# Kernel tuning notes

Measured on AMD Instinct MI355X. Metric: run time of the kernel, lower is better.

The kernel has to match this reference:

```python
import jax, jax.numpy as jnp
import numpy as np

N = 100000
E = 1600000
F_IN = 100
H = 64
C = 18
K = 2  # num_stacks
T = 2  # num_layers


def setup_inputs() -> dict:
    key = jax.random.key(0)
    ks = jax.random.split(key, 12)
    def glorot(k, shape):
        fan = shape[-2] + shape[-1]
        s = jnp.sqrt(6.0 / fan)
        return jax.random.uniform(k, shape, jnp.float32, -s, s)
    return {
        "x": jax.random.normal(ks[0], (N, F_IN), jnp.float32),
        "edge_index": jax.random.randint(ks[1], (2, E), 0, N, jnp.int64),
        "init_w1": glorot(ks[2], (K, F_IN, H)),
        "w1": glorot(ks[3], (K, H, H)),
        "root_w1": glorot(ks[4], (K, F_IN, H)),
        "b1": jnp.zeros((K, 1, H), jnp.float32),
        "init_w2": glorot(ks[5], (K, H, C)),
        "w2": glorot(ks[6], (K, C, C)),
        "root_w2": glorot(ks[7], (K, H, C)),
        "b2": jnp.zeros((K, 1, C), jnp.float32),
    }


def _gcn_norm(src, tgt):
    # symmetric normalization, no self loops (PyG ARMAConv default)
    deg = jax.ops.segment_sum(jnp.ones((E,), jnp.float32), tgt, num_segments=N)
    dis = jnp.where(deg > 0, jax.lax.rsqrt(jnp.maximum(deg, 1.0)), 0.0)
    return dis[src] * dis[tgt]  # [E]


def _arma_conv(x, src, tgt, norm, init_w, w, root_w, b):
    # x: [N, Fin]; returns [N, Fout]
    root = jnp.einsum('nf,kfh->knh', x, root_w)  # [K, N, Fout] (shared across layers)
    out = None
    for t in range(T):
        if t == 0:
            h = jnp.einsum('nf,kfh->knh', x, init_w)
        else:
            h = jnp.einsum('knh,khg->kng', out, w)
        # gather-scale-scatter propagation per stack
        msgs = h[:, src, :] * norm[None, :, None]  # [K, E, Fout]
        agg = jax.vmap(lambda m: jax.ops.segment_sum(m, tgt, num_segments=N))(msgs)
        out = jax.nn.relu(agg + root + b)
    return out.mean(axis=0)  # mean over stacks


def reference(x, edge_index, init_w1, w1, root_w1, b1, init_w2, w2, root_w2, b2):
    src, tgt = edge_index[0], edge_index[1]
    norm = _gcn_norm(src, tgt)
    h = jax.nn.relu(_arma_conv(x, src, tgt, norm, init_w1, w1, root_w1, b1))
    out = _arma_conv(h, src, tgt, norm, init_w2, w2, root_w2, b2)
    return jax.nn.log_softmax(out, axis=-1)
```

## Files before the change

kernel.cpp:

```cpp
#include <hip/hip_runtime.h>
#include <hip/hip_bf16.h>
#include <math.h>

#define N_NODES 100000
#define N_EDGES 1600000
#define F_IN 100
#define H 64
#define C 18
#define BSHIFT 8
#define BSIZE 256
#define NBUCKETS ((N_NODES + BSIZE - 1) >> BSHIFT)
#define NBLK 256
#define CHUNK (N_EDGES / NBLK)

typedef __attribute__((ext_vector_type(8))) short v8s;
typedef __attribute__((ext_vector_type(4))) float v4f;
typedef __attribute__((ext_vector_type(2))) float v2f;


__device__ __forceinline__ unsigned bf16_rne(float f) {
    unsigned u = __float_as_uint(f);
    return (u + 0x7FFFu + ((u >> 16) & 1u)) >> 16;
}
__device__ __forceinline__ unsigned pack_bf2(float a, float b) {
    return bf16_rne(a) | (bf16_rne(b) << 16);
}
__device__ __forceinline__ float2 unpack_bf2(unsigned u) {
    return make_float2(__uint_as_float(u << 16), __uint_as_float(u & 0xFFFF0000u));
}
__device__ __forceinline__ ushort pack_fp8x2(float a, float b) {
    int r = __builtin_amdgcn_cvt_pk_fp8_f32(a, b, 0, false);
    return (ushort)(r & 0xFFFF);
}
__device__ __forceinline__ float2 unpack_fp8x2(ushort u) {
    v2f r = __builtin_amdgcn_cvt_pk_f32_fp8((int)u, false);
    return make_float2(r[0], r[1]);
}


__global__ void scan1_kernel(const int* __restrict__ cnt, int* __restrict__ excl,
                             int* __restrict__ bsum, int n) {
    __shared__ int tmp[256];
    int t = threadIdx.x;
    int i = blockIdx.x * 256 + t;
    int v = (i < n) ? cnt[i] : 0;
    tmp[t] = v;
    __syncthreads();
    for (int off = 1; off < 256; off <<= 1) {
        int xv = (t >= off) ? tmp[t - off] : 0;
        __syncthreads();
        tmp[t] += xv;
        __syncthreads();
    }
    if (i < n) excl[i] = tmp[t] - v;
    if (t == 255) bsum[blockIdx.x] = tmp[255];
}

__global__ void __launch_bounds__(512) scan2p_prep_kernel(
        int* __restrict__ bsum, int nb,
        const float* __restrict__ iw1, const float* __restrict__ rw1,
        const float* __restrict__ w1,  const float* __restrict__ iw2,
        const float* __restrict__ rw2, const float* __restrict__ w2,
        ushort* __restrict__ W1T, ushort* __restrict__ WmT,
        ushort* __restrict__ W2T, ushort* __restrict__ W3T) {
    int t = threadIdx.x;
    if (blockIdx.x == 0) {
        __shared__ int s[512];
        int v = (t < nb) ? bsum[t] : 0;
        s[t] = v;
        __syncthreads();
        for (int off = 1; off < 512; off <<= 1) {
            int xv = (t >= off) ? s[t - off] : 0;
            __syncthreads();
            s[t] += xv;
            __syncthreads();
        }
        if (t < nb) bsum[t] = s[t] - v;
        return;
    }
    int gid = (blockIdx.x - 1) * 512 + t;
    if (gid < 32768) {
        int idx = gid;
        int m = idx >> 13, nn = (idx >> 7) & 63, kk = idx & 127;
        int stk = m & 1, isWr = m >> 1;
        float v = 0.f;
        if (kk < F_IN) v = (isWr ? rw1 : iw1)[((size_t)stk * F_IN + kk) * 64 + nn];
        W1T[idx] = (ushort)bf16_rne(v);
    } else if (gid < 32768 + 8192) {
        int idx = gid - 32768;
        int stk = idx >> 12, g = (idx >> 6) & 63, f = idx & 63;
        WmT[idx] = (ushort)bf16_rne(w1[((size_t)stk * 64 + f) * 64 + g]);
    } else if (gid < 32768 + 8192 + 8192) {
        int idx = gid - 32768 - 8192;
        int m = idx >> 11, col = (idx >> 6) & 31, k = idx & 63;
        int stk = m & 1, isWr = m >> 1;
        float v = 0.f;
        if (col < C) v = (isWr ? rw2 : iw2)[((size_t)stk * H + k) * C + col];
        W2T[idx] = (ushort)bf16_rne(v);
    } else if (gid < 32768 + 8192 + 8192 + 2048) {
        int idx = gid - 32768 - 8192 - 8192;
        int stk = idx >> 10, col = (idx >> 5) & 31, k = idx & 31;
        float v = 0.f;
        if (col < C && k < C) v = w2[((size_t)stk * C + k) * C + col];
        W3T[idx] = (ushort)bf16_rne(v);
    }
}

__global__ void scan3_kernel(int* __restrict__ arr, const int* __restrict__ bsum,
                             int n, int sent) {
    int i = blockIdx.x * 256 + threadIdx.x;
    if (i < n) arr[i] += bsum[i >> 8];
    if (i == n && sent >= 0) arr[n] = sent;
}


__global__ void __launch_bounds__(256) histA_kernel(const int* __restrict__ tgt,
                                                    int* __restrict__ hist) {
    __shared__ int h[NBUCKETS];
    int blk = blockIdx.x, t = threadIdx.x;
    for (int i = t; i < NBUCKETS; i += 256) h[i] = 0;
    __syncthreads();
    int e0 = blk * CHUNK, e1 = e0 + CHUNK;
    for (int e = e0 + t; e < e1; e += 256) atomicAdd(&h[tgt[e] >> BSHIFT], 1);
    __syncthreads();
    for (int i = t; i < NBUCKETS; i += 256) hist[i * NBLK + blk] = h[i];
}

__global__ void __launch_bounds__(256) scatterC_kernel(
        const int* __restrict__ src, const int* __restrict__ tgt,
        const int* __restrict__ histx, unsigned* __restrict__ tmp) {
    __shared__ int cur[NBUCKETS];
    int blk = blockIdx.x, t = threadIdx.x;
    for (int i = t; i < NBUCKETS; i += 256) cur[i] = histx[i * NBLK + blk];
    __syncthreads();
    int e0 = blk * CHUNK, e1 = e0 + CHUNK;
    for (int e = e0 + t; e < e1; e += 256) {
        int s = src[e], tg = tgt[e];
        int b = tg >> BSHIFT;
        int pos = atomicAdd(&cur[b], 1);
        tmp[pos] = (unsigned)s | ((unsigned)(tg & (BSIZE - 1)) << 17);
    }
}

__global__ void __launch_bounds__(256) bucketD2_kernel(
        const unsigned* __restrict__ tmp, const int* __restrict__ histx,
        int* __restrict__ rp, float* __restrict__ dinv, int* __restrict__ ssrc) {
    __shared__ int cnt_l[BSIZE];
    __shared__ int scan_l[BSIZE];
    int b = blockIdx.x;
    int t = threadIdx.x;
    int e_lo = histx[(size_t)b * NBLK];
    int e_hi = (b + 1 < NBUCKETS) ? histx[(size_t)(b + 1) * NBLK] : N_EDGES;
    int n_lo = b << BSHIFT;
    int n_hi = min(n_lo + BSIZE, N_NODES);
    int nn = n_hi - n_lo;
    cnt_l[t] = 0;
    __syncthreads();
    for (int e = e_lo + t; e < e_hi; e += 256)
        atomicAdd(&cnt_l[(int)(tmp[e] >> 17)], 1);
    __syncthreads();
    int v = cnt_l[t];
    scan_l[t] = v;
    __syncthreads();
    for (int off = 1; off < 256; off <<= 1) {
        int xv = (t >= off) ? scan_l[t - off] : 0;
        __syncthreads();
        scan_l[t] += xv;
        __syncthreads();
    }
    int my_start = e_lo + scan_l[t] - v;
    if (t < nn) {
        rp[n_lo + t] = my_start;
        dinv[n_lo + t] = (v > 0) ? rsqrtf((float)v) : 0.f;
    }
    if (b == NBUCKETS - 1 && t == 0) rp[N_NODES] = N_EDGES;
    __syncthreads();
    cnt_l[t] = my_start;
    __syncthreads();
    for (int e = e_lo + t; e < e_hi; e += 256) {
        unsigned p = tmp[e];
        int s = (int)(p & 0x1FFFFu);
        int tl = (int)(p >> 17);
        int pos = atomicAdd(&cnt_l[tl], 1);
        ssrc[pos] = s;
    }
}


__global__ void __launch_bounds__(256) dense1_mfma(
        const float* __restrict__ x, const ushort* __restrict__ W1T,
        const float* __restrict__ dinv,
        ushort* __restrict__ g, unsigned* __restrict__ root) {
    __shared__ char xs[64 * 256];
    int tid = threadIdx.x;
    int b0 = blockIdx.x * 64;
    for (int i = tid; i < 4096; i += 256) {
        int row = i >> 6, pr = i & 63;
        int grow = b0 + row;
        unsigned pv = 0;
        if (grow < N_NODES && 2 * pr < F_IN) {
            float v0 = x[(size_t)grow * F_IN + 2 * pr];
            float v1 = (2 * pr + 1 < F_IN) ? x[(size_t)grow * F_IN + 2 * pr + 1] : 0.f;
            pv = pack_bf2(v0, v1);
        }
        int gr = (pr >> 2) ^ (row & 7);
        *(unsigned*)(xs + row * 256 + (gr << 4) + (pr & 3) * 4) = pv;
    }
    __syncthreads();
    int lane = tid & 63;
    int w = __builtin_amdgcn_readfirstlane(tid >> 6);
    int q = lane >> 4, cl = lane & 15;
    int isWr = w >> 1;
    int colbase = (w & 1) * 32;
    v8s bfr[2][2][4];
    #pragma unroll
    for (int stk = 0; stk < 2; ++stk)
        #pragma unroll
        for (int nt = 0; nt < 2; ++nt)
            #pragma unroll
            for (int ks = 0; ks < 4; ++ks) {
                const ushort* p = W1T + ((size_t)(isWr * 2 + stk) * 64 + colbase + nt * 16 + cl) * 128
                                  + ks * 32 + q * 8;
                bfr[stk][nt][ks] = *(const v8s*)p;
            }
    #pragma unroll
    for (int mt = 0; mt < 4; ++mt) {
        v8s afr[4];
        #pragma unroll
        for (int ks = 0; ks < 4; ++ks) {
            int row = mt * 16 + cl;
            int gr = (ks * 4 + q) ^ (row & 7);
            afr[ks] = *(const v8s*)(xs + row * 256 + (gr << 4));
        }
        v4f acc[2][2];
        #pragma unroll
        for (int stk = 0; stk < 2; ++stk)
            #pragma unroll
            for (int nt = 0; nt < 2; ++nt) {
                v4f a = {0.f, 0.f, 0.f, 0.f};
                #pragma unroll
                for (int ks = 0; ks < 4; ++ks)
                    a = __builtin_amdgcn_mfma_f32_16x16x32_bf16(afr[ks], bfr[stk][nt][ks], a, 0, 0, 0);
                acc[stk][nt] = a;
            }
        #pragma unroll
        for (int nt = 0; nt < 2; ++nt)
            #pragma unroll
            for (int reg = 0; reg < 4; ++reg) {
                int node = b0 + mt * 16 + q * 4 + reg;
                if (node < N_NODES) {
                    int col = colbase + nt * 16 + cl;
                    if (isWr == 0) {
                        float dv = dinv[node];
                        g[(size_t)node * 64 + col] = pack_fp8x2(dv * acc[0][nt][reg], dv * acc[1][nt][reg]);
                    } else {
                        root[(size_t)node * 64 + col] = pack_bf2(acc[0][nt][reg], acc[1][nt][reg]);
                    }
                }
            }
    }
}

__global__ void __launch_bounds__(256) dense_mid_mfma(
        const ushort* __restrict__ hk0, const ushort* __restrict__ hk1,
        const ushort* __restrict__ WmT, const float* __restrict__ dinv,
        ushort* __restrict__ g2) {
    __shared__ char hs[2 * 64 * 128];
    int tid = threadIdx.x;
    int b0 = blockIdx.x * 64;
    for (int i = tid; i < 1024; i += 256) {
        int stk = i >> 9, rem = i & 511, row = rem >> 3, gr = rem & 7;
        int grow = b0 + row;
        uint4 v = make_uint4(0, 0, 0, 0);
        const ushort* srcp = stk ? hk1 : hk0;
        if (grow < N_NODES) v = *(const uint4*)(srcp + (size_t)grow * 64 + gr * 8);
        *(uint4*)(hs + stk * 8192 + row * 128 + ((gr ^ (row & 7)) << 4)) = v;
    }
    __syncthreads();
    int lane = tid & 63;
    int w = __builtin_amdgcn_readfirstlane(tid >> 6);
    int q = lane >> 4, cl = lane & 15;
    v8s bfr[2][2];
    #pragma unroll
    for (int stk = 0; stk < 2; ++stk)
        #pragma unroll
        for (int ks = 0; ks < 2; ++ks)
            bfr[stk][ks] = *(const v8s*)(WmT + ((size_t)stk * 64 + w * 16 + cl) * 64 + ks * 32 + q * 8);
    #pragma unroll
    for (int mt = 0; mt < 4; ++mt) {
        v4f acc[2];
        #pragma unroll
        for (int stk = 0; stk < 2; ++stk) {
            v4f a = {0.f, 0.f, 0.f, 0.f};
            #pragma unroll
            for (int ks = 0; ks < 2; ++ks) {
                int row = mt * 16 + cl;
                int gr = (ks * 4 + q) ^ (row & 7);
                v8s af = *(const v8s*)(hs + stk * 8192 + row * 128 + (gr << 4));
                a = __builtin_amdgcn_mfma_f32_16x16x32_bf16(af, bfr[stk][ks], a, 0, 0, 0);
            }
            acc[stk] = a;
        }
        #pragma unroll
        for (int reg = 0; reg < 4; ++reg) {
            int node = b0 + mt * 16 + q * 4 + reg;
            if (node < N_NODES) {
                float dv = dinv[node];
                g2[(size_t)node * 64 + w * 16 + cl] = pack_fp8x2(dv * acc[0][reg], dv * acc[1][reg]);
            }
        }
    }
}

__global__ void __launch_bounds__(256) dense_y2_mfma(
        const ushort* __restrict__ yb, const ushort* __restrict__ W2T,
        const float* __restrict__ dinv,
        unsigned* __restrict__ h2, unsigned* __restrict__ root2) {
    __shared__ char ys[64 * 128];
    int tid = threadIdx.x;
    int b0 = blockIdx.x * 64;
    for (int i = tid; i < 512; i += 256) {
        int row = i >> 3, gr = i & 7;
        int grow = b0 + row;
        uint4 v = make_uint4(0, 0, 0, 0);
        if (grow < N_NODES) v = *(const uint4*)(yb + (size_t)grow * 64 + gr * 8);
        *(uint4*)(ys + row * 128 + ((gr ^ (row & 7)) << 4)) = v;
    }
    __syncthreads();
    int lane = tid & 63;
    int w = __builtin_amdgcn_readfirstlane(tid >> 6);
    int q = lane >> 4, cl = lane & 15;
    int isWr = w >> 1;
    int mbase = (w & 1) * 2;
    v8s bfr[2][2][2];
    #pragma unroll
    for (int stk = 0; stk < 2; ++stk)
        #pragma unroll
        for (int nt = 0; nt < 2; ++nt)
            #pragma unroll
            for (int ks = 0; ks < 2; ++ks)
                bfr[stk][nt][ks] = *(const v8s*)(W2T + ((size_t)(isWr * 2 + stk) * 32 + nt * 16 + cl) * 64
                                                 + ks * 32 + q * 8);
    #pragma unroll
    for (int mi = 0; mi < 2; ++mi) {
        int mt = mbase + mi;
        v8s afr[2];
        #pragma unroll
        for (int ks = 0; ks < 2; ++ks) {
            int row = mt * 16 + cl;
            int gr = (ks * 4 + q) ^ (row & 7);
            afr[ks] = *(const v8s*)(ys + row * 128 + (gr << 4));
        }
        v4f acc[2][2];
        #pragma unroll
        for (int stk = 0; stk < 2; ++stk)
            #pragma unroll
            for (int nt = 0; nt < 2; ++nt) {
                v4f a = {0.f, 0.f, 0.f, 0.f};
                #pragma unroll
                for (int ks = 0; ks < 2; ++ks)
                    a = __builtin_amdgcn_mfma_f32_16x16x32_bf16(afr[ks], bfr[stk][nt][ks], a, 0, 0, 0);
                acc[stk][nt] = a;
            }
        #pragma unroll
        for (int nt = 0; nt < 2; ++nt)
            #pragma unroll
            for (int reg = 0; reg < 4; ++reg) {
                int node = b0 + mt * 16 + q * 4 + reg;
                int col = nt * 16 + cl;
                if (node < N_NODES && col < C) {
                    if (isWr == 0) {
                        float dv = dinv[node];
                        h2[(size_t)node * C + col] = pack_bf2(dv * acc[0][nt][reg], dv * acc[1][nt][reg]);
                    } else {
                        root2[(size_t)node * C + col] = pack_bf2(acc[0][nt][reg], acc[1][nt][reg]);
                    }
                }
            }
    }
}

__global__ void __launch_bounds__(256) dense_last_mfma(
        const ushort* __restrict__ ok0, const ushort* __restrict__ ok1,
        const ushort* __restrict__ W3T, const float* __restrict__ dinv,
        unsigned* __restrict__ h3) {
    __shared__ char hs[2 * 64 * 64];
    int tid = threadIdx.x;
    int b0 = blockIdx.x * 64;
    for (int i = tid; i < 2048; i += 256) ((unsigned*)hs)[i] = 0;
    __syncthreads();
    for (int i = tid; i < 4096; i += 256) {
        int stk = i >> 11, row = (i >> 5) & 63, col = i & 31;
        int node = b0 + row;
        if (col < C && node < N_NODES) {
            ushort v = (stk ? ok1 : ok0)[(size_t)node * C + col];
            int gr = (col >> 3) ^ (row & 3);
            *(ushort*)(hs + stk * 4096 + row * 64 + (gr << 4) + (col & 7) * 2) = v;
        }
    }
    __syncthreads();
    int lane = tid & 63;
    int w = __builtin_amdgcn_readfirstlane(tid >> 6);
    int q = lane >> 4, cl = lane & 15;
    v8s bfr[2][2];
    #pragma unroll
    for (int stk = 0; stk < 2; ++stk)
        #pragma unroll
        for (int nt = 0; nt < 2; ++nt)
            bfr[stk][nt] = *(const v8s*)(W3T + ((size_t)stk * 32 + nt * 16 + cl) * 32 + q * 8);
    int row = w * 16 + cl;
    int gr = q ^ (row & 3);
    v8s af0 = *(const v8s*)(hs + row * 64 + (gr << 4));
    v8s af1 = *(const v8s*)(hs + 4096 + row * 64 + (gr << 4));
    v4f acc[2][2];
    #pragma unroll
    for (int nt = 0; nt < 2; ++nt) {
        acc[0][nt] = __builtin_amdgcn_mfma_f32_16x16x32_bf16(af0, bfr[0][nt], (v4f){0.f,0.f,0.f,0.f}, 0, 0, 0);
        acc[1][nt] = __builtin_amdgcn_mfma_f32_16x16x32_bf16(af1, bfr[1][nt], (v4f){0.f,0.f,0.f,0.f}, 0, 0, 0);
    }
    #pragma unroll
    for (int nt = 0; nt < 2; ++nt)
        #pragma unroll
        for (int reg = 0; reg < 4; ++reg) {
            int node = b0 + w * 16 + q * 4 + reg;
            int col = nt * 16 + cl;
            if (node < N_NODES && col < C) {
                float dv = dinv[node];
                h3[(size_t)node * C + col] = pack_bf2(dv * acc[0][nt][reg], dv * acc[1][nt][reg]);
            }
        }
}


template <int FINAL>
__global__ void __launch_bounds__(256) prop64_kernel(
        const ushort* __restrict__ g, const unsigned* __restrict__ root,
        const float* __restrict__ b, const float* __restrict__ dinv,
        const int* __restrict__ rp, const int* __restrict__ ssrc,
        ushort* __restrict__ ok0, ushort* __restrict__ ok1, ushort* __restrict__ yb) {
    int lane = threadIdx.x & 63;
    int wid = __builtin_amdgcn_readfirstlane((int)((blockIdx.x * 256 + threadIdx.x) >> 6));
    if (wid >= N_NODES) return;
    int e0 = rp[wid], e1 = rp[wid + 1];
    float a0 = 0.f, a1 = 0.f;
    int e = e0;
    for (; e + 8 <= e1; e += 8) {
        ushort u[8];
        #pragma unroll
        for (int j = 0; j < 8; ++j) u[j] = g[(size_t)ssrc[e + j] * H + lane];
        #pragma unroll
        for (int j = 0; j < 8; ++j) { float2 v = unpack_fp8x2(u[j]); a0 += v.x; a1 += v.y; }
    }
    for (; e < e1; ++e) {
        float2 v = unpack_fp8x2(g[(size_t)ssrc[e] * H + lane]);
        a0 += v.x; a1 += v.y;
    }
    float dv = dinv[wid];
    float2 rt = unpack_bf2(root[(size_t)wid * H + lane]);
    float o0 = fmaxf(fmaf(dv, a0, rt.x + b[lane]), 0.f);
    float o1 = fmaxf(fmaf(dv, a1, rt.y + b[H + lane]), 0.f);
    if (FINAL) {
        yb[(size_t)wid * H + lane] = (ushort)bf16_rne(0.5f * (o0 + o1));
    } else {
        ok0[(size_t)wid * H + lane] = (ushort)bf16_rne(o0);
        ok1[(size_t)wid * H + lane] = (ushort)bf16_rne(o1);
    }
}

template <int FINAL>
__global__ void __launch_bounds__(256) prop18_kernel(
        const unsigned* __restrict__ g, const unsigned* __restrict__ root,
        const float* __restrict__ b, const float* __restrict__ dinv,
        const int* __restrict__ rp, const int* __restrict__ ssrc,
        ushort* __restrict__ ok0, ushort* __restrict__ ok1, float* __restrict__ outp) {
    int lane = threadIdx.x & 63;
    int wid = __builtin_amdgcn_readfirstlane((int)((blockIdx.x * 256 + threadIdx.x) >> 6));
    if (wid >= N_NODES) return;
    int e0 = rp[wid], e1 = rp[wid + 1];
    bool act = lane < C;
    int c = act ? lane : 0;
    float a0 = 0.f, a1 = 0.f;
    int e = e0;
    for (; e + 8 <= e1; e += 8) {
        unsigned u[8];
        #pragma unroll
        for (int j = 0; j < 8; ++j) u[j] = g[(size_t)ssrc[e + j] * C + c];
        if (act) {
            #pragma unroll
            for (int j = 0; j < 8; ++j) { float2 v = unpack_bf2(u[j]); a0 += v.x; a1 += v.y; }
        }
    }
    for (; e < e1; ++e) {
        float2 v = unpack_bf2(g[(size_t)ssrc[e] * C + c]);
        if (act) { a0 += v.x; a1 += v.y; }
    }
    float dv = dinv[wid];
    if (!FINAL) {
        if (act) {
            float2 rt = unpack_bf2(root[(size_t)wid * C + c]);
            float o0 = fmaxf(fmaf(dv, a0, rt.x + b[c]), 0.f);
            float o1 = fmaxf(fmaf(dv, a1, rt.y + b[C + c]), 0.f);
            ok0[(size_t)wid * C + c] = (ushort)bf16_rne(o0);
            ok1[(size_t)wid * C + c] = (ushort)bf16_rne(o1);
        }
    } else {
        float m = -INFINITY;
        if (act) {
            float2 rt = unpack_bf2(root[(size_t)wid * C + c]);
            float o0 = fmaxf(fmaf(dv, a0, rt.x + b[c]), 0.f);
            float o1 = fmaxf(fmaf(dv, a1, rt.y + b[C + c]), 0.f);
            m = 0.5f * (o0 + o1);
        }
        float mx = m;
        #pragma unroll
        for (int off = 16; off >= 1; off >>= 1) mx = fmaxf(mx, __shfl_xor(mx, off, 64));
        float ex = act ? __expf(m - mx) : 0.f;
        float sum = ex;
        #pragma unroll
        for (int off = 16; off >= 1; off >>= 1) sum += __shfl_xor(sum, off, 64);
        if (act) outp[(size_t)wid * C + c] = m - mx - logf(sum);
    }
}


extern "C" void kernel_launch(void* const* d_in, const int* in_sizes, int n_in,
                              void* d_out, int out_size, void* d_ws, size_t ws_size,
                              hipStream_t stream) {
    const float* x        = (const float*)d_in[0];
    const int*   ei       = (const int*)d_in[1];
    const float* init_w1  = (const float*)d_in[2];
    const float* w1       = (const float*)d_in[3];
    const float* root_w1  = (const float*)d_in[4];
    const float* b1       = (const float*)d_in[5];
    const float* init_w2  = (const float*)d_in[6];
    const float* w2       = (const float*)d_in[7];
    const float* root_w2  = (const float*)d_in[8];
    const float* b2       = (const float*)d_in[9];
    const int* src = ei;
    const int* tgt = ei + N_EDGES;
    float* out = (float*)d_out;

    char* w = (char*)d_ws;
    size_t off = 0;
    auto alloc = [&](size_t bytes) -> char* {
        char* p = w + off;
        off += (bytes + 255) & ~(size_t)255;
        return p;
    };
    int*      rp    = (int*)alloc((size_t)(N_NODES + 1) * 4);
    float*    dinv  = (float*)alloc((size_t)N_NODES * 4);
    int*      bsum  = (int*)alloc(512 * 4);
    int*      hist  = (int*)alloc((size_t)NBUCKETS * NBLK * 4);
    int*      histx = (int*)alloc((size_t)NBUCKETS * NBLK * 4);
    unsigned* tmp   = (unsigned*)alloc((size_t)N_EDGES * 4);
    int*      ssrc  = (int*)alloc((size_t)N_EDGES * 4);
    ushort*   W1T   = (ushort*)alloc((size_t)4 * 64 * 128 * 2);
    ushort*   WmT   = (ushort*)alloc((size_t)2 * 64 * 64 * 2);
    ushort*   W2T   = (ushort*)alloc((size_t)4 * 32 * 64 * 2);
    ushort*   W3T   = (ushort*)alloc((size_t)2 * 32 * 32 * 2);
    ushort*   g1    = (ushort*)alloc((size_t)N_NODES * H * 2);
    unsigned* root1 = (unsigned*)alloc((size_t)N_NODES * H * 4);
    ushort*   hk0   = (ushort*)alloc((size_t)N_NODES * H * 2);
    ushort*   hk1   = (ushort*)alloc((size_t)N_NODES * H * 2);
    ushort*   g2    = (ushort*)alloc((size_t)N_NODES * H * 2);
    ushort*   yb    = (ushort*)alloc((size_t)N_NODES * H * 2);
    unsigned* l2buf = (unsigned*)alloc((size_t)3 * N_NODES * C * 4);
    unsigned* h2u    = l2buf;
    unsigned* root2u = l2buf + (size_t)N_NODES * C;
    unsigned* h3u    = l2buf + (size_t)2 * N_NODES * C;
    ushort*   p18k0  = (ushort*)root1;
    ushort*   p18k1  = (ushort*)root1 + (size_t)N_NODES * C;

    int nbH = (NBUCKETS * NBLK + 255) / 256;

    histA_kernel<<<NBLK, 256, 0, stream>>>(tgt, hist);
    scan1_kernel<<<nbH, 256, 0, stream>>>(hist, histx, bsum, NBUCKETS * NBLK);
    scan2p_prep_kernel<<<101, 512, 0, stream>>>(bsum, nbH,
                                                init_w1, root_w1, w1, init_w2, root_w2, w2,
                                                W1T, WmT, W2T, W3T);
    scan3_kernel<<<nbH, 256, 0, stream>>>(histx, bsum, NBUCKETS * NBLK, -1);
    scatterC_kernel<<<NBLK, 256, 0, stream>>>(src, tgt, histx, tmp);
    bucketD2_kernel<<<NBUCKETS, 256, 0, stream>>>(tmp, histx, rp, dinv, ssrc);

    int gblocks = (N_NODES + 63) / 64;
    int pgrid   = (N_NODES + 3) / 4;

    dense1_mfma<<<gblocks, 256, 0, stream>>>(x, W1T, dinv, g1, root1);
    prop64_kernel<0><<<pgrid, 256, 0, stream>>>(g1, root1, b1, dinv, rp, ssrc, hk0, hk1, nullptr);
    dense_mid_mfma<<<gblocks, 256, 0, stream>>>(hk0, hk1, WmT, dinv, g2);
    prop64_kernel<1><<<pgrid, 256, 0, stream>>>(g2, root1, b1, dinv, rp, ssrc, nullptr, nullptr, yb);

    dense_y2_mfma<<<gblocks, 256, 0, stream>>>(yb, W2T, dinv, h2u, root2u);
    prop18_kernel<0><<<pgrid, 256, 0, stream>>>(h2u, root2u, b2, dinv, rp, ssrc, p18k0, p18k1, nullptr);
    dense_last_mfma<<<gblocks, 256, 0, stream>>>(p18k0, p18k1, W3T, dinv, h3u);
    prop18_kernel<1><<<pgrid, 256, 0, stream>>>(h3u, root2u, b2, dinv, rp, ssrc, nullptr, nullptr, out);
}
```

Before: 332.0 us.

## Store 18-wide layer-2 messages as fp8 pairs and split edges across half-waves

```diff
diff --git a/kernel.cpp b/kernel.cpp
--- a/kernel.cpp
+++ b/kernel.cpp
@@ -315,7 +315,7 @@
 __global__ void __launch_bounds__(256) dense_y2_mfma(
         const ushort* __restrict__ yb, const ushort* __restrict__ W2T,
         const float* __restrict__ dinv,
-        unsigned* __restrict__ h2, unsigned* __restrict__ root2) {
+        ushort* __restrict__ h2, unsigned* __restrict__ root2) {
     __shared__ char ys[64 * 128];
     int tid = threadIdx.x;
     int b0 = blockIdx.x * 64;
@@ -371,7 +371,7 @@
                 if (node < N_NODES && col < C) {
                     if (isWr == 0) {
                         float dv = dinv[node];
-                        h2[(size_t)node * C + col] = pack_bf2(dv * acc[0][nt][reg], dv * acc[1][nt][reg]);
+                        h2[(size_t)node * C + col] = pack_fp8x2(dv * acc[0][nt][reg], dv * acc[1][nt][reg]);
                     } else {
                         root2[(size_t)node * C + col] = pack_bf2(acc[0][nt][reg], acc[1][nt][reg]);
                     }
@@ -383,7 +383,7 @@
 __global__ void __launch_bounds__(256) dense_last_mfma(
         const ushort* __restrict__ ok0, const ushort* __restrict__ ok1,
         const ushort* __restrict__ W3T, const float* __restrict__ dinv,
-        unsigned* __restrict__ h3) {
+        ushort* __restrict__ h3) {
     __shared__ char hs[2 * 64 * 64];
     int tid = threadIdx.x;
     int b0 = blockIdx.x * 64;
@@ -426,7 +426,7 @@
             int col = nt * 16 + cl;
             if (node < N_NODES && col < C) {
                 float dv = dinv[node];
-                h3[(size_t)node * C + col] = pack_bf2(dv * acc[0][nt][reg], dv * acc[1][nt][reg]);
+                h3[(size_t)node * C + col] = pack_fp8x2(dv * acc[0][nt][reg], dv * acc[1][nt][reg]);
             }
         }
 }
@@ -469,7 +469,7 @@
 
 template <int FINAL>
 __global__ void __launch_bounds__(256) prop18_kernel(
-        const unsigned* __restrict__ g, const unsigned* __restrict__ root,
+        const ushort* __restrict__ g, const unsigned* __restrict__ root,
         const float* __restrict__ b, const float* __restrict__ dinv,
         const int* __restrict__ rp, const int* __restrict__ ssrc,
         ushort* __restrict__ ok0, ushort* __restrict__ ok1, float* __restrict__ outp) {
@@ -477,26 +477,31 @@
     int wid = __builtin_amdgcn_readfirstlane((int)((blockIdx.x * 256 + threadIdx.x) >> 6));
     if (wid >= N_NODES) return;
     int e0 = rp[wid], e1 = rp[wid + 1];
-    bool act = lane < C;
-    int c = act ? lane : 0;
+    int half = lane >> 5;
+    int c32 = lane & 31;
+    bool actG = c32 < C;
+    int c = actG ? c32 : 0;
     float a0 = 0.f, a1 = 0.f;
-    int e = e0;
-    for (; e + 8 <= e1; e += 8) {
-        unsigned u[8];
-        #pragma unroll
-        for (int j = 0; j < 8; ++j) u[j] = g[(size_t)ssrc[e + j] * C + c];
-        if (act) {
-            #pragma unroll
-            for (int j = 0; j < 8; ++j) { float2 v = unpack_bf2(u[j]); a0 += v.x; a1 += v.y; }
-        }
-    }
-    for (; e < e1; ++e) {
-        float2 v = unpack_bf2(g[(size_t)ssrc[e] * C + c]);
-        if (act) { a0 += v.x; a1 += v.y; }
-    }
+    int e = e0 + half;
+    for (; e + 16 <= e1; e += 16) {
+        ushort u[8];
+        #pragma unroll
+        for (int j = 0; j < 8; ++j) u[j] = g[(size_t)ssrc[e + 2 * j] * C + c];
+        if (actG) {
+            #pragma unroll
+            for (int j = 0; j < 8; ++j) { float2 v = unpack_fp8x2(u[j]); a0 += v.x; a1 += v.y; }
+        }
+    }
+    for (; e < e1; e += 2) {
+        float2 v = unpack_fp8x2(g[(size_t)ssrc[e] * C + c]);
+        if (actG) { a0 += v.x; a1 += v.y; }
+    }
+    a0 += __shfl_xor(a0, 32, 64);
+    a1 += __shfl_xor(a1, 32, 64);
     float dv = dinv[wid];
+    bool actO = lane < C;
     if (!FINAL) {
-        if (act) {
+        if (actO) {
             float2 rt = unpack_bf2(root[(size_t)wid * C + c]);
             float o0 = fmaxf(fmaf(dv, a0, rt.x + b[c]), 0.f);
             float o1 = fmaxf(fmaf(dv, a1, rt.y + b[C + c]), 0.f);
@@ -505,7 +510,7 @@
         }
     } else {
         float m = -INFINITY;
-        if (act) {
+        if (actO) {
             float2 rt = unpack_bf2(root[(size_t)wid * C + c]);
             float o0 = fmaxf(fmaf(dv, a0, rt.x + b[c]), 0.f);
             float o1 = fmaxf(fmaf(dv, a1, rt.y + b[C + c]), 0.f);
@@ -514,11 +519,11 @@
         float mx = m;
         #pragma unroll
         for (int off = 16; off >= 1; off >>= 1) mx = fmaxf(mx, __shfl_xor(mx, off, 64));
-        float ex = act ? __expf(m - mx) : 0.f;
+        float ex = actO ? __expf(m - mx) : 0.f;
         float sum = ex;
         #pragma unroll
         for (int off = 16; off >= 1; off >>= 1) sum += __shfl_xor(sum, off, 64);
-        if (act) outp[(size_t)wid * C + c] = m - mx - logf(sum);
+        if (actO) outp[(size_t)wid * C + c] = m - mx - logf(sum);
     }
 }
 
@@ -564,12 +569,11 @@
     ushort*   hk1   = (ushort*)alloc((size_t)N_NODES * H * 2);
     ushort*   g2    = (ushort*)alloc((size_t)N_NODES * H * 2);
     ushort*   yb    = (ushort*)alloc((size_t)N_NODES * H * 2);
-    unsigned* l2buf = (unsigned*)alloc((size_t)3 * N_NODES * C * 4);
-    unsigned* h2u    = l2buf;
-    unsigned* root2u = l2buf + (size_t)N_NODES * C;
-    unsigned* h3u    = l2buf + (size_t)2 * N_NODES * C;
-    ushort*   p18k0  = (ushort*)root1;
-    ushort*   p18k1  = (ushort*)root1 + (size_t)N_NODES * C;
+    ushort*   h2u   = (ushort*)alloc((size_t)N_NODES * C * 2);
+    unsigned* root2u= (unsigned*)alloc((size_t)N_NODES * C * 4);
+    ushort*   h3u   = (ushort*)alloc((size_t)N_NODES * C * 2);
+    ushort*   p18k0 = (ushort*)root1;
+    ushort*   p18k1 = (ushort*)root1 + (size_t)N_NODES * C;
 
     int nbH = (NBUCKETS * NBLK + 255) / 256;
 
```

Result: slower. 349.8 us (+5.3%).
